# Kernel tuning notes

Hardware: AMD Instinct MI355X
Metric: run time of the kernel (lower is better)

Reference implementation:

```python
import jax, jax.numpy as jnp
import numpy as np

D_MODEL = 1024
NUM_HEADS = 16
D_K = D_MODEL // NUM_HEADS


def setup_inputs() -> dict:
    key = jax.random.key(0)
    ks = jax.random.split(key, 9)
    B, T = 4, 2048
    s = 0.02
    return {
        "x": jax.random.normal(ks[0], (B, T, D_MODEL), dtype=jnp.float32),
        "wq": jax.random.normal(ks[1], (D_MODEL, D_MODEL), dtype=jnp.float32) * s,
        "bq": jax.random.normal(ks[2], (D_MODEL,), dtype=jnp.float32) * s,
        "wk": jax.random.normal(ks[3], (D_MODEL, D_MODEL), dtype=jnp.float32) * s,
        "bk": jax.random.normal(ks[4], (D_MODEL,), dtype=jnp.float32) * s,
        "wv": jax.random.normal(ks[5], (D_MODEL, D_MODEL), dtype=jnp.float32) * s,
        "bv": jax.random.normal(ks[6], (D_MODEL,), dtype=jnp.float32) * s,
        "wo": jax.random.normal(ks[7], (D_MODEL, D_MODEL), dtype=jnp.float32) * s,
        "bo": jax.random.normal(ks[8], (D_MODEL,), dtype=jnp.float32) * s,
    }


def reference(x, wq, bq, wk, bk, wv, bv, wo, bo):
    B, T, D = x.shape
    H, dk = NUM_HEADS, D_K
    # Linear projections (torch Linear: x @ W.T + b; here weights stored as [D_in, D_out])
    q = (x @ wq + bq).reshape(B, T, H, dk).transpose(0, 2, 1, 3)  # [B,H,T,dk]
    k = (x @ wk + bk).reshape(B, T, H, dk).transpose(0, 2, 1, 3)
    v = (x @ wv + bv).reshape(B, T, H, dk).transpose(0, 2, 1, 3)
    scale = 1.0 / jnp.sqrt(jnp.asarray(dk, x.dtype))
    scores = jnp.einsum('bhqd,bhkd->bhqk', q, k) * scale  # [B,H,T,T]
    causal = jnp.tril(jnp.ones((T, T), dtype=bool))
    scores = jnp.where(causal[None, None], scores, jnp.asarray(-jnp.inf, scores.dtype))
    probs = jax.nn.softmax(scores, axis=-1)
    y = jnp.einsum('bhqk,bhkd->bhqd', probs, v)  # [B,H,T,dk]
    y = y.transpose(0, 2, 1, 3).reshape(B, T, D)
    return y @ wo + bo
```

## Files before the change

### kernel.cpp

```cpp
#include <hip/hip_runtime.h>
#include <hip/hip_bf16.h>
#include <stdint.h>

typedef __attribute__((ext_vector_type(8))) short bf16x8;
typedef __attribute__((ext_vector_type(4))) float f32x4;
typedef __hip_bfloat16 bf16_t;

#define D_MODEL 1024
#define NHEADS  16
#define DK      64
#define TSEQ    2048
#define BATCH   4
#define MTOK    (BATCH*TSEQ)

#define QSCALE 0.18033688011112042f

#define FSWZ(r) ((((r) & 3)) | ((((r) >> 3) & 1) << 2))

typedef __attribute__((address_space(3))) uint32_t lds_u32;
typedef const __attribute__((address_space(1))) uint32_t glb_u32;

__device__ __forceinline__ void load_lds16(const void* g, void* l) {
    __builtin_amdgcn_global_load_lds((glb_u32*)g, (lds_u32*)l, 16, 0, 0);
}

__global__ __launch_bounds__(256) void convert_x_kernel(const float* __restrict__ x,
                                                        bf16_t* __restrict__ out, int n4) {
    int i = blockIdx.x * 256 + threadIdx.x;
    if (i >= n4) return;
    float4 v = reinterpret_cast<const float4*>(x)[i];
    union { bf16_t h[4]; uint2 u; } p;
    p.h[0] = __float2bfloat16(v.x);
    p.h[1] = __float2bfloat16(v.y);
    p.h[2] = __float2bfloat16(v.z);
    p.h[3] = __float2bfloat16(v.w);
    reinterpret_cast<uint2*>(out)[i] = p.u;
}

__global__ __launch_bounds__(256) void transpose_w_kernel(
    const float* __restrict__ w0, const float* __restrict__ w1,
    const float* __restrict__ w2, const float* __restrict__ w3,
    bf16_t* __restrict__ o0, bf16_t* __restrict__ o1,
    bf16_t* __restrict__ o2, bf16_t* __restrict__ o3) {
    const float* w = (blockIdx.z == 0) ? w0 : (blockIdx.z == 1) ? w1 : (blockIdx.z == 2) ? w2 : w3;
    bf16_t* o = (blockIdx.z == 0) ? o0 : (blockIdx.z == 1) ? o1 : (blockIdx.z == 2) ? o2 : o3;
    const float wscale = (blockIdx.z == 0) ? QSCALE : 1.0f;
    __shared__ float tile[32][33];
    int tx = threadIdx.x, ty = threadIdx.y;
    int bx = blockIdx.x * 32;
    int by = blockIdx.y * 32;
    #pragma unroll
    for (int i = 0; i < 4; ++i)
        tile[ty + i*8][tx] = w[(bx + ty + i*8) * D_MODEL + by + tx];
    __syncthreads();
    #pragma unroll
    for (int i = 0; i < 4; ++i)
        o[(by + ty + i*8) * D_MODEL + bx + tx] = __float2bfloat16(tile[tx][ty + i*8] * wscale);
}

template<int FINAL>
__global__ __launch_bounds__(256) void gemm_staged_kernel(
    const bf16_t* __restrict__ A, const bf16_t* __restrict__ BtBase,
    const float* __restrict__ bias0, const float* __restrict__ bias1,
    const float* __restrict__ bias2, void* __restrict__ Cb) {
    const int K = D_MODEL;
    const int tid = threadIdx.x;
    const int wave = tid >> 6, lane = tid & 63;
    const int wm = wave >> 1, wn = wave & 1;
    const int mt = blockIdx.y * 128;
    const int nt = blockIdx.x * 128;
    const int m0 = mt + wm * 64;
    const int n0 = nt + wn * 64;
    const int z = FINAL ? 0 : blockIdx.z;
    const bf16_t* Bt = BtBase + (size_t)z * (D_MODEL * D_MODEL);
    const float* bias = FINAL ? bias0 : (z == 0 ? bias0 : z == 1 ? bias1 : bias2);
    const float bscale = (!FINAL && z == 0) ? QSCALE : 1.0f;
    const int lr = lane & 15, lg = lane >> 4;

    __shared__ __align__(16) bf16_t Atile[128 * 64];
    __shared__ __align__(16) bf16_t Btile[128 * 64];

    const int srow = wave * 32 + (lane >> 3);
    const int sl = (lane & 7) ^ (lane >> 3);
    const size_t asrc0 = (size_t)(mt + srow) * K + sl * 8;
    const size_t bsrc0 = (size_t)(nt + srow) * K + sl * 8;

    f32x4 acc[4][4] = {};
    #pragma unroll 1
    for (int k0 = 0; k0 < K; k0 += 64) {
        __syncthreads();
        #pragma unroll
        for (int i = 0; i < 4; ++i) {
            char* adst = (char*)Atile + wave * 4096 + i * 1024;
            char* bdst = (char*)Btile + wave * 4096 + i * 1024;
            load_lds16(A  + asrc0 + (size_t)i * 8 * K + k0, adst);
            load_lds16(Bt + bsrc0 + (size_t)i * 8 * K + k0, bdst);
        }
        __syncthreads();
        #pragma unroll
        for (int kk = 0; kk < 2; ++kk) {
            bf16x8 a[4], b[4];
            #pragma unroll
            for (int mi = 0; mi < 4; ++mi) {
                const int row = wm * 64 + mi * 16 + lr;
                a[mi] = *reinterpret_cast<const bf16x8*>(
                    (const char*)Atile + row * 128 + (((kk * 4 + lg) ^ (lr & 7)) * 16));
            }
            #pragma unroll
            for (int ni = 0; ni < 4; ++ni) {
                const int row = wn * 64 + ni * 16 + lr;
                b[ni] = *reinterpret_cast<const bf16x8*>(
                    (const char*)Btile + row * 128 + (((kk * 4 + lg) ^ (lr & 7)) * 16));
            }
            #pragma unroll
            for (int mi = 0; mi < 4; ++mi)
                #pragma unroll
                for (int ni = 0; ni < 4; ++ni)
                    acc[mi][ni] = __builtin_amdgcn_mfma_f32_16x16x32_bf16(a[mi], b[ni], acc[mi][ni], 0, 0, 0);
        }
    }
    #pragma unroll
    for (int mi = 0; mi < 4; ++mi) {
        #pragma unroll
        for (int ni = 0; ni < 4; ++ni) {
            const int col = n0 + ni * 16 + lr;
            const float bv = bias[col] * bscale;
            #pragma unroll
            for (int r = 0; r < 4; ++r) {
                const int row = m0 + mi * 16 + lg * 4 + r;
                const float val = acc[mi][ni][r] + bv;
                if (FINAL) {
                    reinterpret_cast<float*>(Cb)[(size_t)row * D_MODEL + col] = val;
                } else if (z <= 1) {
                    size_t idx = (size_t)z * (MTOK * D_MODEL) +
                        (((size_t)(row >> 11) * NHEADS + (col >> 6)) * TSEQ + (row & 2047)) * DK + (col & 63);
                    reinterpret_cast<bf16_t*>(Cb)[idx] = __float2bfloat16(val);
                } else {
                    size_t idx = (size_t)2 * (MTOK * D_MODEL) +
                        (((size_t)(row >> 11) * NHEADS + (col >> 6)) * DK + (col & 63)) * TSEQ + (row & 2047);
                    reinterpret_cast<bf16_t*>(Cb)[idx] = __float2bfloat16(val);
                }
            }
        }
    }
}

__global__ __launch_bounds__(512) void attn_kernel(
    const bf16_t* __restrict__ Q, const bf16_t* __restrict__ K,
    const bf16_t* __restrict__ Vt, bf16_t* __restrict__ Y) {
    const int qpair = blockIdx.x;
    const int bh = blockIdx.y;
    const int tid = threadIdx.x;
    const int wave = tid >> 6, lane = tid & 63;
    const int lr = lane & 15, lg = lane >> 4;

    const bf16_t* Qh = Q + (size_t)bh * TSEQ * DK;
    const bf16_t* Kh = K + (size_t)bh * TSEQ * DK;
    const bf16_t* Vh = Vt + (size_t)bh * DK * TSEQ;

    __shared__ __align__(16) char smem[2][16384];

    const int srow = tid >> 3;
    const int sslot = (tid & 7) ^ FSWZ(srow);
    const size_t koff = (size_t)srow * DK + sslot * 8;
    const size_t voff = (size_t)srow * TSEQ + sslot * 8;

    const int rbase = (lr >> 2) * 8 + (lr & 3);
    const int bcast = (lane & 48) | (lg * 4);

    #pragma unroll 1
    for (int tt = 0; tt < 2; ++tt) {
        const int j = tt ? (15 - qpair) : qpair;
        const int NT = 2 * j + 2;
        const int q0 = j * 128 + wave * 16;

        bf16x8 qf[2];
        #pragma unroll
        for (int kk = 0; kk < 2; ++kk)
            qf[kk] = *reinterpret_cast<const bf16x8*>(&Qh[(size_t)(q0 + lr) * DK + kk*32 + lg*8]);

        f32x4 o[4] = {};
        float mrun = -__builtin_inff();
        float lrun = 0.f;

        int cur = 0;
        load_lds16(Kh + koff, smem[0] + wave * 1024);
        load_lds16(Vh + voff, smem[0] + 8192 + wave * 1024);

        #pragma unroll 1
        for (int kt = 0; kt < NT; ++kt) {
            if (kt + 1 < NT) {
                load_lds16(Kh + (size_t)(kt + 1) * 64 * DK + koff, smem[cur ^ 1] + wave * 1024);
                load_lds16(Vh + (size_t)(kt + 1) * 64 + voff, smem[cur ^ 1] + 8192 + wave * 1024);
                asm volatile("s_waitcnt vmcnt(2)" ::: "memory");
            } else {
                asm volatile("s_waitcnt vmcnt(0)" ::: "memory");
            }
            __builtin_amdgcn_s_barrier();
            __builtin_amdgcn_sched_barrier(0);

            if (kt * 64 <= q0 + 15) {
                const char* kb = smem[cur];
                f32x4 s[4] = {};
                #pragma unroll
                for (int fk = 0; fk < 4; ++fk) {
                    const int krow = (fk >> 1)*32 + (fk & 1)*4 + rbase;
                    #pragma unroll
                    for (int kk = 0; kk < 2; ++kk) {
                        const bf16x8 kv = *reinterpret_cast<const bf16x8*>(
                            kb + krow*128 + (((kk*4 + lg) ^ FSWZ(krow)) * 16));
                        s[fk] = __builtin_amdgcn_mfma_f32_16x16x32_bf16(kv, qf[kk], s[fk], 0, 0, 0);
                    }
                }
                if (kt * 64 + 63 > q0) {
                    const int qrow = q0 + lr;
                    #pragma unroll
                    for (int fk = 0; fk < 4; ++fk) {
                        const int kb0 = kt*64 + (fk >> 1)*32 + lg*8 + (fk & 1)*4;
                        #pragma unroll
                        for (int r = 0; r < 4; ++r)
                            if (kb0 + r > qrow) s[fk][r] = -__builtin_inff();
                    }
                }
                float tmax = s[0][0];
                #pragma unroll
                for (int fk = 0; fk < 4; ++fk)
                    #pragma unroll
                    for (int r = 0; r < 4; ++r)
                        tmax = fmaxf(tmax, s[fk][r]);
                tmax = fmaxf(tmax, __shfl_xor(tmax, 16, 64));
                tmax = fmaxf(tmax, __shfl_xor(tmax, 32, 64));
                if (__any(tmax - mrun > 11.5f)) {
                    const float mnew = fmaxf(mrun, tmax);
                    const float alpha = exp2f(mrun - mnew);
                    mrun = mnew;
                    lrun *= alpha;
                    #pragma unroll
                    for (int r = 0; r < 4; ++r) {
                        const float ar = __shfl(alpha, bcast + r, 64);
                        #pragma unroll
                        for (int fn = 0; fn < 4; ++fn)
                            o[fn][r] *= ar;
                    }
                }
                float tsum = 0.f;
                #pragma unroll
                for (int fk = 0; fk < 4; ++fk)
                    #pragma unroll
                    for (int r = 0; r < 4; ++r) {
                        const float p = exp2f(s[fk][r] - mrun);
                        s[fk][r] = p;
                        tsum += p;
                    }
                tsum += __shfl_xor(tsum, 16, 64);
                tsum += __shfl_xor(tsum, 32, 64);
                lrun += tsum;
                union { bf16x8 v; bf16_t h[8]; } pa[2];
                #pragma unroll
                for (int c = 0; c < 2; ++c)
                    #pragma unroll
                    for (int jj = 0; jj < 8; ++jj)
                        pa[c].h[jj] = __float2bfloat16(s[2*c + (jj >> 2)][jj & 3]);
                #pragma unroll
                for (int fn = 0; fn < 4; ++fn) {
                    const int vrow = fn*16 + lr;
                    #pragma unroll
                    for (int c = 0; c < 2; ++c) {
                        const bf16x8 vv = *reinterpret_cast<const bf16x8*>(
                            kb + 8192 + vrow*128 + (((c*4 + lg) ^ FSWZ(vrow)) * 16));
                        o[fn] = __builtin_amdgcn_mfma_f32_16x16x32_bf16(pa[c].v, vv, o[fn], 0, 0, 0);
                    }
                }
            }
            __builtin_amdgcn_sched_barrier(0);
            __builtin_amdgcn_s_barrier();
            cur ^= 1;
        }

        const int b = bh >> 4, h = bh & 15;
        #pragma unroll
        for (int r = 0; r < 4; ++r) {
            const float lsum = __shfl(lrun, bcast + r, 64);
            const float inv = 1.f / lsum;
            const int t = q0 + lg*4 + r;
            #pragma unroll
            for (int fn = 0; fn < 4; ++fn)
                Y[(((size_t)b * TSEQ + t) * NHEADS + h) * DK + fn*16 + lr] =
                    __float2bfloat16(o[fn][r] * inv);
        }
    }
}

extern "C" void kernel_launch(void* const* d_in, const int* in_sizes, int n_in,
                              void* d_out, int out_size, void* d_ws, size_t ws_size,
                              hipStream_t stream) {
    const float* x  = (const float*)d_in[0];
    const float* wq = (const float*)d_in[1];
    const float* bq = (const float*)d_in[2];
    const float* wk = (const float*)d_in[3];
    const float* bk = (const float*)d_in[4];
    const float* wv = (const float*)d_in[5];
    const float* bv = (const float*)d_in[6];
    const float* wo = (const float*)d_in[7];
    const float* bo = (const float*)d_in[8];
    float* out = (float*)d_out;

    char* ws = (char*)d_ws;
    const size_t MB = 1u << 20;
    bf16_t* xb  = (bf16_t*)(ws);
    bf16_t* Yb  = (bf16_t*)(ws);
    bf16_t* wqt = (bf16_t*)(ws + 16*MB);
    bf16_t* wkt = (bf16_t*)(ws + 18*MB);
    bf16_t* wvt = (bf16_t*)(ws + 20*MB);
    bf16_t* wot = (bf16_t*)(ws + 22*MB);
    bf16_t* Qb  = (bf16_t*)(ws + 24*MB);
    bf16_t* Kb  = (bf16_t*)(ws + 40*MB);
    bf16_t* Vtb = (bf16_t*)(ws + 56*MB);

    const int n4 = (MTOK * D_MODEL) / 4;
    convert_x_kernel<<<(n4 + 255) / 256, 256, 0, stream>>>(x, xb, n4);
    transpose_w_kernel<<<dim3(32, 32, 4), dim3(32, 8), 0, stream>>>(
        wq, wk, wv, wo, wqt, wkt, wvt, wot);

    gemm_staged_kernel<0><<<dim3(D_MODEL / 128, MTOK / 128, 3), 256, 0, stream>>>(
        xb, wqt, bq, bk, bv, Qb);

    attn_kernel<<<dim3(8, BATCH * NHEADS), 512, 0, stream>>>(Qb, Kb, Vtb, Yb);

    gemm_staged_kernel<1><<<dim3(D_MODEL / 128, MTOK / 128, 1), 256, 0, stream>>>(
        Yb, wot, bo, nullptr, nullptr, out);
}
```

Before: 292.5 us.

## Double-buffer GEMM LDS tiles and remap blocks for XCD-local L2 reuse

```diff
diff --git a/kernel.cpp b/kernel.cpp
--- a/kernel.cpp
+++ b/kernel.cpp
@@ -67,18 +67,26 @@
     const int tid = threadIdx.x;
     const int wave = tid >> 6, lane = tid & 63;
     const int wm = wave >> 1, wn = wave & 1;
-    const int mt = blockIdx.y * 128;
-    const int nt = blockIdx.x * 128;
+
+    const int flat = blockIdx.x + 8 * (blockIdx.y + 64 * blockIdx.z);
+    const int xcd = flat & 7;
+    const int idx = flat >> 3;
+    const int bx  = idx & 7;
+    const int byl = (idx >> 3) & 7;
+    const int z   = FINAL ? 0 : (idx >> 6);
+    const int by  = xcd * 8 + byl;
+
+    const int mt = by * 128;
+    const int nt = bx * 128;
     const int m0 = mt + wm * 64;
     const int n0 = nt + wn * 64;
-    const int z = FINAL ? 0 : blockIdx.z;
     const bf16_t* Bt = BtBase + (size_t)z * (D_MODEL * D_MODEL);
     const float* bias = FINAL ? bias0 : (z == 0 ? bias0 : z == 1 ? bias1 : bias2);
     const float bscale = (!FINAL && z == 0) ? QSCALE : 1.0f;
     const int lr = lane & 15, lg = lane >> 4;
 
-    __shared__ __align__(16) bf16_t Atile[128 * 64];
-    __shared__ __align__(16) bf16_t Btile[128 * 64];
+    __shared__ __align__(16) bf16_t Atile[2][128 * 64];
+    __shared__ __align__(16) bf16_t Btile[2][128 * 64];
 
     const int srow = wave * 32 + (lane >> 3);
     const int sl = (lane & 7) ^ (lane >> 3);
@@ -86,17 +94,30 @@
     const size_t bsrc0 = (size_t)(nt + srow) * K + sl * 8;
 
     f32x4 acc[4][4] = {};
+    int cur = 0;
+    #pragma unroll
+    for (int i = 0; i < 4; ++i) {
+        load_lds16(A  + asrc0 + (size_t)i * 8 * K, (char*)Atile[0] + wave * 4096 + i * 1024);
+        load_lds16(Bt + bsrc0 + (size_t)i * 8 * K, (char*)Btile[0] + wave * 4096 + i * 1024);
+    }
+
     #pragma unroll 1
     for (int k0 = 0; k0 < K; k0 += 64) {
-        __syncthreads();
-        #pragma unroll
-        for (int i = 0; i < 4; ++i) {
-            char* adst = (char*)Atile + wave * 4096 + i * 1024;
-            char* bdst = (char*)Btile + wave * 4096 + i * 1024;
-            load_lds16(A  + asrc0 + (size_t)i * 8 * K + k0, adst);
-            load_lds16(Bt + bsrc0 + (size_t)i * 8 * K + k0, bdst);
-        }
-        __syncthreads();
+        if (k0 + 64 < K) {
+            #pragma unroll
+            for (int i = 0; i < 4; ++i) {
+                load_lds16(A  + asrc0 + (size_t)i * 8 * K + k0 + 64,
+                           (char*)Atile[cur ^ 1] + wave * 4096 + i * 1024);
+                load_lds16(Bt + bsrc0 + (size_t)i * 8 * K + k0 + 64,
+                           (char*)Btile[cur ^ 1] + wave * 4096 + i * 1024);
+            }
+            asm volatile("s_waitcnt vmcnt(8)" ::: "memory");
+        } else {
+            asm volatile("s_waitcnt vmcnt(0)" ::: "memory");
+        }
+        __builtin_amdgcn_s_barrier();
+        __builtin_amdgcn_sched_barrier(0);
+
         #pragma unroll
         for (int kk = 0; kk < 2; ++kk) {
             bf16x8 a[4], b[4];
@@ -104,13 +125,13 @@
             for (int mi = 0; mi < 4; ++mi) {
                 const int row = wm * 64 + mi * 16 + lr;
                 a[mi] = *reinterpret_cast<const bf16x8*>(
-                    (const char*)Atile + row * 128 + (((kk * 4 + lg) ^ (lr & 7)) * 16));
+                    (const char*)Atile[cur] + row * 128 + (((kk * 4 + lg) ^ (lr & 7)) * 16));
             }
             #pragma unroll
             for (int ni = 0; ni < 4; ++ni) {
                 const int row = wn * 64 + ni * 16 + lr;
                 b[ni] = *reinterpret_cast<const bf16x8*>(
-                    (const char*)Btile + row * 128 + (((kk * 4 + lg) ^ (lr & 7)) * 16));
+                    (const char*)Btile[cur] + row * 128 + (((kk * 4 + lg) ^ (lr & 7)) * 16));
             }
             #pragma unroll
             for (int mi = 0; mi < 4; ++mi)
@@ -118,6 +139,9 @@
                 for (int ni = 0; ni < 4; ++ni)
                     acc[mi][ni] = __builtin_amdgcn_mfma_f32_16x16x32_bf16(a[mi], b[ni], acc[mi][ni], 0, 0, 0);
         }
+        __builtin_amdgcn_sched_barrier(0);
+        __builtin_amdgcn_s_barrier();
+        cur ^= 1;
     }
     #pragma unroll
     for (int mi = 0; mi < 4; ++mi) {
@@ -132,13 +156,13 @@
                 if (FINAL) {
                     reinterpret_cast<float*>(Cb)[(size_t)row * D_MODEL + col] = val;
                 } else if (z <= 1) {
-                    size_t idx = (size_t)z * (MTOK * D_MODEL) +
+                    size_t idx2 = (size_t)z * (MTOK * D_MODEL) +
                         (((size_t)(row >> 11) * NHEADS + (col >> 6)) * TSEQ + (row & 2047)) * DK + (col & 63);
-                    reinterpret_cast<bf16_t*>(Cb)[idx] = __float2bfloat16(val);
+                    reinterpret_cast<bf16_t*>(Cb)[idx2] = __float2bfloat16(val);
                 } else {
-                    size_t idx = (size_t)2 * (MTOK * D_MODEL) +
+                    size_t idx2 = (size_t)2 * (MTOK * D_MODEL) +
                         (((size_t)(row >> 11) * NHEADS + (col >> 6)) * DK + (col & 63)) * TSEQ + (row & 2047);
-                    reinterpret_cast<bf16_t*>(Cb)[idx] = __float2bfloat16(val);
+                    reinterpret_cast<bf16_t*>(Cb)[idx2] = __float2bfloat16(val);
                 }
             }
         }
```

New measurement: 274.1 us. 1.07x faster.
